# Kernel tuning notes

Measured on AMD Instinct MI355X. Metric: run time of the kernel, lower is better.

Reference implementation:

```python
import jax, jax.numpy as jnp
import numpy as np

N = 50000
E = 800000
H = 128

def _mlp_params(key, sizes, biases):
    # sizes: list of (in, out); biases: list of bool
    params = []
    for i, ((fi, fo), b) in enumerate(zip(sizes, biases)):
        k = jax.random.fold_in(key, i)
        bound = 1.0 / np.sqrt(fi)
        W = jax.random.uniform(k, (fi, fo), minval=-bound, maxval=bound, dtype=jnp.float32)
        if b:
            bb = jax.random.uniform(jax.random.fold_in(k, 7), (fo,), minval=-bound, maxval=bound, dtype=jnp.float32)
        else:
            bb = None
        params.append((W, bb))
    return params

def setup_inputs() -> dict:
    key = jax.random.key(0)
    ks = jax.random.split(key, 8)
    h = jax.random.normal(ks[0], (N, H), dtype=jnp.float32)
    pos = jax.random.normal(ks[1], (N, 3), dtype=jnp.float32)
    edge_index = jax.random.randint(ks[2], (2, E), 0, N, dtype=jnp.int32)
    edge_p = _mlp_params(ks[3], [(2 * H + 1, H), (H, H)], [True, True])
    node_p = _mlp_params(ks[4], [(2 * H, H), (H, H)], [True, True])
    coord_p = _mlp_params(ks[5], [(H, H), (H, 1)], [True, False])
    return {
        'h': h, 'pos': pos, 'edge_index': edge_index,
        'eW0': edge_p[0][0], 'eb0': edge_p[0][1], 'eW1': edge_p[1][0], 'eb1': edge_p[1][1],
        'nW0': node_p[0][0], 'nb0': node_p[0][1], 'nW1': node_p[1][0], 'nb1': node_p[1][1],
        'cW0': coord_p[0][0], 'cb0': coord_p[0][1], 'cW1': coord_p[1][0],
    }

def reference(h, pos, edge_index, eW0, eb0, eW1, eb1, nW0, nb0, nW1, nb1, cW0, cb0, cW1):
    row, col = edge_index[0], edge_index[1]
    coord_diff = pos[row] - pos[col]                         # [E, 3]
    radial = jnp.sum(coord_diff ** 2, axis=1, keepdims=True)  # [E, 1]
    edge_feat = jnp.concatenate([h[row], h[col], radial], axis=1)  # [E, 2H+1]
    # edge MLP: Linear -> SiLU -> Linear -> SiLU
    m_ij = jax.nn.silu(edge_feat @ eW0 + eb0)
    m_ij = jax.nn.silu(m_ij @ eW1 + eb1)                     # [E, H]
    # coord MLP: Linear -> SiLU -> Linear(no bias)
    coord_weight = jax.nn.silu(m_ij @ cW0 + cb0) @ cW1       # [E, 1]
    norm = jnp.sqrt(radial + 1e-8)
    coord_update = coord_diff / norm * coord_weight          # [E, 3]
    # scatter-add messages to target nodes
    m_i = jax.ops.segment_sum(m_ij, row, num_segments=h.shape[0])
    node_in = jnp.concatenate([h, m_i], axis=1)              # [N, 2H]
    h_new = h + jax.nn.silu(node_in @ nW0 + nb0) @ nW1 + nb1
    pos_update = jax.ops.segment_sum(coord_update, row, num_segments=pos.shape[0])
    deg = jax.ops.segment_sum(jnp.ones((row.shape[0],), jnp.float32), row, num_segments=pos.shape[0])
    pos_new = pos + pos_update / (deg[:, None] + 1e-6)
    return h_new, pos_new
```

## Files before the change

kernel.cpp:

```cpp
#include <hip/hip_runtime.h>
#include <hip/hip_bf16.h>
#include <cstddef>

#define N_NODES 50000
#define N_EDGES 800000
#define HDIM    128
#define TME     64
#define TMN     64

#define RB128   272
#define RB256   528

#define SCHUNK  512
#define SNBLK   ((N_NODES + SCHUNK - 1) / SCHUNK)

typedef __attribute__((ext_vector_type(4))) float f32x4;
typedef __attribute__((ext_vector_type(8))) short bf16x8;

#define OFF_EW0T 0
#define OFF_EW0B 16384
#define OFF_EW1  32768
#define OFF_CW0  49152
#define OFF_NW0  65536
#define OFF_NW1  98304
#define PACK_ELEMS 114688

__device__ __forceinline__ float silu(float x) {
    float e = __expf(-x);
    return __fdividef(x, 1.0f + e);
}
__device__ __forceinline__ unsigned short f2bf(float f) {
    union { __hip_bfloat16 h; unsigned short u; } cv;
    cv.h = __float2bfloat16(f);
    return cv.u;
}
__device__ __forceinline__ unsigned int f2bf2(float a, float b) {
    union { __hip_bfloat162 h; unsigned int u; } cv;
    cv.h = __float22bfloat162_rn(float2{a, b});
    return cv.u;
}
__device__ __forceinline__ float bf2f(unsigned short u) {
    return __uint_as_float(((unsigned int)u) << 16);
}
__device__ __forceinline__ float bflo(unsigned int u) {
    return __uint_as_float(u << 16);
}
__device__ __forceinline__ float bfhi(unsigned int u) {
    return __uint_as_float(u & 0xffff0000u);
}

__global__ void pack_weights(const float* __restrict__ eW0, const float* __restrict__ eW1,
                             const float* __restrict__ cW0, const float* __restrict__ nW0,
                             const float* __restrict__ nW1, unsigned short* __restrict__ pack)
{
    int g = blockIdx.x * blockDim.x + threadIdx.x;
    int f = g >> 6;
    int lane = g & 63;
    const float* W; int base; int rowoff = 0;
    if (f < 32)       { W = eW0; base = OFF_EW0T; }
    else if (f < 64)  { W = eW0; base = OFF_EW0B; f -= 32; rowoff = 128; }
    else if (f < 96)  { W = eW1; base = OFF_EW1;  f -= 64; }
    else if (f < 128) { W = cW0; base = OFF_CW0;  f -= 96; }
    else if (f < 192) { W = nW0; base = OFF_NW0;  f -= 128; }
    else              { W = nW1; base = OFF_NW1;  f -= 192; }
    int KS = (base == OFF_NW0) ? 8 : 4;
    int cb = f / KS, ks = f % KS;
    int col = cb * 16 + (lane & 15);
    int kbase = rowoff + ks * 32 + ((lane >> 4) << 3);
#pragma unroll
    for (int j = 0; j < 8; ++j)
        pack[(size_t)base + ((size_t)(f * 64 + lane) * 8 + j)] =
            f2bf(W[(size_t)(kbase + j) * HDIM + col]);
}

__global__ __launch_bounds__(256)
void scanA_kernel(const int* __restrict__ cnt, int* __restrict__ bsum) {
    __shared__ int part[256];
    const int b = blockIdx.x, t = threadIdx.x;
    int i0 = b * SCHUNK + t * 2;
    int s = 0;
    if (i0 < N_NODES)     s += cnt[i0];
    if (i0 + 1 < N_NODES) s += cnt[i0 + 1];
    part[t] = s;
    __syncthreads();
    for (int off = 128; off > 0; off >>= 1) {
        if (t < off) part[t] += part[t + off];
        __syncthreads();
    }
    if (t == 0) bsum[b] = part[0];
}

__global__ __launch_bounds__(128)
void scanB_kernel(const int* __restrict__ bsum, int* __restrict__ boff,
                  int* __restrict__ row_start) {
    __shared__ int part[128];
    const int t = threadIdx.x;
    int s = (t < SNBLK) ? bsum[t] : 0;
    part[t] = s;
    __syncthreads();
    for (int off = 1; off < 128; off <<= 1) {
        int tmp = (t >= off) ? part[t - off] : 0;
        __syncthreads();
        part[t] += tmp;
        __syncthreads();
    }
    boff[t] = part[t] - s;
    if (t == 127) row_start[N_NODES] = part[127];
}

__global__ __launch_bounds__(256)
void scanC_kernel(const int* __restrict__ cnt, const int* __restrict__ boff,
                  int* __restrict__ row_start, int* __restrict__ cursor) {
    __shared__ int part[256];
    const int b = blockIdx.x, t = threadIdx.x;
    int i0 = b * SCHUNK + t * 2;
    int c0 = (i0 < N_NODES) ? cnt[i0] : 0;
    int c1 = (i0 + 1 < N_NODES) ? cnt[i0 + 1] : 0;
    int s = c0 + c1;
    part[t] = s;
    __syncthreads();
    for (int off = 1; off < 256; off <<= 1) {
        int tmp = (t >= off) ? part[t - off] : 0;
        __syncthreads();
        part[t] += tmp;
        __syncthreads();
    }
    int base = boff[b] + part[t] - s;
    if (i0 < N_NODES)     { row_start[i0] = base;          cursor[i0] = base; }
    if (i0 + 1 < N_NODES) { row_start[i0 + 1] = base + c0; cursor[i0 + 1] = base + c0; }
}

__global__ void scatter_kernel(const int* __restrict__ eidx, int* __restrict__ cursor,
                               int2* __restrict__ rc) {
    int e = (blockIdx.x * blockDim.x + threadIdx.x) * 4;
    if (e + 3 < N_EDGES) {
        int4 r4 = *(const int4*)(eidx + e);
        int4 c4 = *(const int4*)(eidx + N_EDGES + e);
        int p;
        p = atomicAdd(&cursor[r4.x], 1); rc[p] = int2{r4.x, c4.x};
        p = atomicAdd(&cursor[r4.y], 1); rc[p] = int2{r4.y, c4.y};
        p = atomicAdd(&cursor[r4.z], 1); rc[p] = int2{r4.z, c4.z};
        p = atomicAdd(&cursor[r4.w], 1); rc[p] = int2{r4.w, c4.w};
    } else {
        for (int i = e; i < N_EDGES; ++i) {
            int r = eidx[i], c = eidx[N_EDGES + i];
            int p = atomicAdd(&cursor[r], 1);
            rc[p] = int2{r, c};
        }
    }
}

template<int KS, int ROWB>
__device__ __forceinline__ void gemm_layer_T(const unsigned short* __restrict__ Wseg,
                                             const char* __restrict__ Xs,
                                             int lane, int cb, f32x4 acc[4])
{
    const bf16x8* aptr = (const bf16x8*)Wseg + (size_t)(cb * KS) * 64 + lane;
#pragma unroll
    for (int ks = 0; ks < KS; ++ks) {
        bf16x8 a = aptr[(size_t)ks * 64];
#pragma unroll
        for (int eb = 0; eb < 4; ++eb) {
            int row = eb * 16 + (lane & 15);
            bf16x8 b = *(const bf16x8*)(Xs + row * ROWB + ks * 64 + ((lane >> 4) << 4));
            acc[eb] = __builtin_amdgcn_mfma_f32_16x16x32_bf16(a, b, acc[eb], 0, 0, 0);
        }
    }
}

__global__ __launch_bounds__(512, 2)
void h0_kernel(const float* __restrict__ h, const float* __restrict__ eb0,
               const unsigned short* __restrict__ pack,
               const int* __restrict__ eidx, int* __restrict__ cnt,
               unsigned short* __restrict__ H0r, unsigned short* __restrict__ H0c)
{
    __shared__ __align__(16) char Xs[TMN * RB128];
    const int tid = threadIdx.x, lane = tid & 63, cb = tid >> 6;
    const int n0 = blockIdx.x * TMN;

    {
        int e = blockIdx.x * 1024 + tid * 2;
        if (e + 1 < N_EDGES) {
            int2 rr = *(const int2*)(eidx + e);
            atomicAdd(&cnt[rr.x], 1);
            atomicAdd(&cnt[rr.y], 1);
        } else if (e < N_EDGES) {
            atomicAdd(&cnt[eidx[e]], 1);
        }
    }

    {
        const int nl = tid >> 3, sub = tid & 7, n = n0 + nl;
        if (n < N_NODES) {
            const float4* h4 = (const float4*)(h + (size_t)n * HDIM);
#pragma unroll
            for (int q = 0; q < 4; ++q) {
                float4 f = h4[sub + q * 8];
                uint2 u; u.x = f2bf2(f.x, f.y); u.y = f2bf2(f.z, f.w);
                *(uint2*)(Xs + nl * RB128 + (sub + q * 8) * 8) = u;
            }
        } else {
            uint2 z{0, 0};
#pragma unroll
            for (int q = 0; q < 4; ++q)
                *(uint2*)(Xs + nl * RB128 + (sub + q * 8) * 8) = z;
        }
    }
    __syncthreads();

    const int j0 = cb * 16 + ((lane >> 4) << 2);
    f32x4 acc[4];
    {
        float4 b0 = *(const float4*)(eb0 + j0);
#pragma unroll
        for (int eb = 0; eb < 4; ++eb) acc[eb] = f32x4{b0.x, b0.y, b0.z, b0.w};
        gemm_layer_T<4, RB128>(pack + OFF_EW0T, Xs, lane, cb, acc);
#pragma unroll
        for (int eb = 0; eb < 4; ++eb) {
            int n = n0 + eb * 16 + (lane & 15);
            if (n < N_NODES) {
                uint2 u; u.x = f2bf2(acc[eb][0], acc[eb][1]); u.y = f2bf2(acc[eb][2], acc[eb][3]);
                *(uint2*)(H0r + (size_t)n * HDIM + j0) = u;
            }
        }
    }
    {
#pragma unroll
        for (int eb = 0; eb < 4; ++eb) acc[eb] = f32x4{0.f, 0.f, 0.f, 0.f};
        gemm_layer_T<4, RB128>(pack + OFF_EW0B, Xs, lane, cb, acc);
#pragma unroll
        for (int eb = 0; eb < 4; ++eb) {
            int n = n0 + eb * 16 + (lane & 15);
            if (n < N_NODES) {
                uint2 u; u.x = f2bf2(acc[eb][0], acc[eb][1]); u.y = f2bf2(acc[eb][2], acc[eb][3]);
                *(uint2*)(H0c + (size_t)n * HDIM + j0) = u;
            }
        }
    }
}

__global__ __launch_bounds__(512, 4)
void egnn_edge_kernel(const unsigned short* __restrict__ H0r,
                      const unsigned short* __restrict__ H0c,
                      const float* __restrict__ pos,
                      const int2*  __restrict__ rc,
                      const float* __restrict__ w256,
                      const float* __restrict__ eb1, const float* __restrict__ cb0,
                      const float* __restrict__ cW1,
                      const unsigned short* __restrict__ pack,
                      float* __restrict__ m_i,
                      float* __restrict__ pos_upd)
{
    __shared__ __align__(16) char Ya[TME * RB128];
    __shared__ __align__(16) char Yb[TME * RB128];
    __shared__ float pw[8][TME];
    __shared__ float rad_s[TME];
    __shared__ float dif_s[TME][3];
    __shared__ float cu_s[TME][4];
    __shared__ int   rowb_s[TME];

    const int tid = threadIdx.x, lane = tid & 63, cb = tid >> 6;

    int lb;
    {
        const int nwg = gridDim.x;
        const int q = nwg >> 3, r = nwg & 7;
        const int xcd = blockIdx.x & 7, idx = blockIdx.x >> 3;
        lb = (xcd < r) ? (xcd * (q + 1) + idx) : (r * (q + 1) + (xcd - r) * q + idx);
    }
    const int e0 = lb * TME;

    {
        const int el = tid >> 3, sub = tid & 7, idx = e0 + el;
        const int2 rcv = rc[idx];
        const int r = rcv.x, c = rcv.y;
        float dx = pos[(size_t)r * 3 + 0] - pos[(size_t)c * 3 + 0];
        float dy = pos[(size_t)r * 3 + 1] - pos[(size_t)c * 3 + 1];
        float dz = pos[(size_t)r * 3 + 2] - pos[(size_t)c * 3 + 2];
        float rad = dx * dx + dy * dy + dz * dz;
        if (sub == 0) {
            rad_s[el] = rad;
            dif_s[el][0] = dx; dif_s[el][1] = dy; dif_s[el][2] = dz;
            rowb_s[el] = r;
        }
        const bf16x8* ar = (const bf16x8*)(H0r + (size_t)r * HDIM + sub * 16);
        const bf16x8* ac = (const bf16x8*)(H0c + (size_t)c * HDIM + sub * 16);
        bf16x8 a0 = ar[0], a1 = ar[1];
        bf16x8 c0 = ac[0], c1 = ac[1];
        const float4* wp = (const float4*)(w256 + sub * 16);
        float4 w4[4] = { wp[0], wp[1], wp[2], wp[3] };
        const float* wf = (const float*)w4;
        float v[16];
#pragma unroll
        for (int i = 0; i < 8; ++i) v[i]     = bf2f((unsigned short)a0[i]) + bf2f((unsigned short)c0[i]);
#pragma unroll
        for (int i = 0; i < 8; ++i) v[8 + i] = bf2f((unsigned short)a1[i]) + bf2f((unsigned short)c1[i]);
#pragma unroll
        for (int i = 0; i < 16; ++i) v[i] = silu(fmaf(rad, wf[i], v[i]));
#pragma unroll
        for (int c4 = 0; c4 < 4; ++c4) {
            uint2 u;
            u.x = f2bf2(v[c4 * 4 + 0], v[c4 * 4 + 1]);
            u.y = f2bf2(v[c4 * 4 + 2], v[c4 * 4 + 3]);
            *(uint2*)(Ya + el * RB128 + sub * 32 + c4 * 8) = u;
        }
    }
    __syncthreads();

    const int j0 = cb * 16 + ((lane >> 4) << 2);
    f32x4 acc[4];

    {
        float4 b1 = *(const float4*)(eb1 + j0);
#pragma unroll
        for (int eb = 0; eb < 4; ++eb) acc[eb] = f32x4{b1.x, b1.y, b1.z, b1.w};
        gemm_layer_T<4, RB128>(pack + OFF_EW1, Ya, lane, cb, acc);
#pragma unroll
        for (int eb = 0; eb < 4; ++eb) {
            int e = eb * 16 + (lane & 15);
            float s0 = silu(acc[eb][0]), s1 = silu(acc[eb][1]);
            float s2 = silu(acc[eb][2]), s3 = silu(acc[eb][3]);
            uint2 u; u.x = f2bf2(s0, s1); u.y = f2bf2(s2, s3);
            *(uint2*)(Yb + e * RB128 + j0 * 2) = u;
        }
    }
    __syncthreads();

    {
        const int rcol = tid & 127;
        const int ch   = tid >> 7;
        float run = 0.f;
        int cur = rowb_s[ch * 16];
#pragma unroll
        for (int i = 0; i < 16; ++i) {
            int row = ch * 16 + i;
            int rr = rowb_s[row];
            if (rr != cur) {
                atomicAdd(&m_i[(size_t)cur * HDIM + rcol], run);
                run = 0.f; cur = rr;
            }
            unsigned short u = *(const unsigned short*)(Yb + row * RB128 + rcol * 2);
            run += bf2f(u);
        }
        atomicAdd(&m_i[(size_t)cur * HDIM + rcol], run);
    }

    {
        float4 b2 = *(const float4*)(cb0 + j0);
#pragma unroll
        for (int eb = 0; eb < 4; ++eb) acc[eb] = f32x4{b2.x, b2.y, b2.z, b2.w};
        gemm_layer_T<4, RB128>(pack + OFF_CW0, Yb, lane, cb, acc);
        float4 w1 = *(const float4*)(cW1 + j0);
        float pe[4];
#pragma unroll
        for (int eb = 0; eb < 4; ++eb) {
            float p;
            p = silu(acc[eb][0]) * w1.x;
            p = fmaf(silu(acc[eb][1]), w1.y, p);
            p = fmaf(silu(acc[eb][2]), w1.z, p);
            p = fmaf(silu(acc[eb][3]), w1.w, p);
            p += __shfl_xor(p, 16);
            p += __shfl_xor(p, 32);
            pe[eb] = p;
        }
        if (lane < 16) {
#pragma unroll
            for (int eb = 0; eb < 4; ++eb) pw[cb][eb * 16 + lane] = pe[eb];
        }
    }
    __syncthreads();

    if (tid < TME) {
        float s = 0.f;
#pragma unroll
        for (int w = 0; w < 8; ++w) s += pw[w][tid];
        float inv = 1.0f / sqrtf(rad_s[tid] + 1e-8f);
        float cwv = s * inv;
        cu_s[tid][0] = dif_s[tid][0] * cwv;
        cu_s[tid][1] = dif_s[tid][1] * cwv;
        cu_s[tid][2] = dif_s[tid][2] * cwv;
    }
    __syncthreads();

    if (tid < TME) {
        const int el = tid;
        bool head = (el == 0) || (rowb_s[el] != rowb_s[el - 1]);
        if (head) {
            float sx = 0.f, sy = 0.f, sz = 0.f;
            int r = rowb_s[el];
            int j = el;
            do {
                sx += cu_s[j][0]; sy += cu_s[j][1]; sz += cu_s[j][2];
                ++j;
            } while (j < TME && rowb_s[j] == r);
            atomicAdd(&pos_upd[(size_t)r * 3 + 0], sx);
            atomicAdd(&pos_upd[(size_t)r * 3 + 1], sy);
            atomicAdd(&pos_upd[(size_t)r * 3 + 2], sz);
        }
    }
}

__global__ __launch_bounds__(512)
void egnn_node_kernel(const float* __restrict__ h,
                      const float* __restrict__ pos,
                      const float* __restrict__ m_i,
                      const float* __restrict__ pos_upd,
                      const int*   __restrict__ row_start,
                      const float* __restrict__ nb0, const float* __restrict__ nb1,
                      const unsigned short* __restrict__ pack,
                      float* __restrict__ out_h,
                      float* __restrict__ out_pos)
{
    __shared__ __align__(16) char Xs[TMN * RB256];
    __shared__ __align__(16) char Ya[TMN * RB128];

    const int tid = threadIdx.x, lane = tid & 63, cb = tid >> 6;
    const int n0 = blockIdx.x * TMN;

    if (tid < TMN * 3) {
        int nl = tid / 3, d = tid % 3;
        int n = n0 + nl;
        if (n < N_NODES) {
            float dv = (float)(row_start[n + 1] - row_start[n]);
            out_pos[(size_t)n * 3 + d] =
                pos[(size_t)n * 3 + d] + pos_upd[(size_t)n * 3 + d] / (dv + 1e-6f);
        }
    }

    {
        const int nl = tid >> 3, sub = tid & 7, n = n0 + nl;
        if (n < N_NODES) {
            const float4* h4 = (const float4*)(h   + (size_t)n * HDIM);
            const float4* m4 = (const float4*)(m_i + (size_t)n * HDIM);
#pragma unroll
            for (int q = 0; q < 4; ++q) {
                float4 fh = h4[sub + q * 8];
                float4 fm = m4[sub + q * 8];
                uint2 uh; uh.x = f2bf2(fh.x, fh.y); uh.y = f2bf2(fh.z, fh.w);
                uint2 um; um.x = f2bf2(fm.x, fm.y); um.y = f2bf2(fm.z, fm.w);
                *(uint2*)(Xs + nl * RB256 + (sub + q * 8) * 8)       = uh;
                *(uint2*)(Xs + nl * RB256 + 256 + (sub + q * 8) * 8) = um;
            }
        } else {
            uint2 z{0, 0};
#pragma unroll
            for (int q = 0; q < 4; ++q) {
                *(uint2*)(Xs + nl * RB256 + (sub + q * 8) * 8)       = z;
                *(uint2*)(Xs + nl * RB256 + 256 + (sub + q * 8) * 8) = z;
            }
        }
    }
    __syncthreads();

    const int j0 = cb * 16 + ((lane >> 4) << 2);
    f32x4 acc[4];

    {
        float4 b0 = *(const float4*)(nb0 + j0);
#pragma unroll
        for (int eb = 0; eb < 4; ++eb) acc[eb] = f32x4{b0.x, b0.y, b0.z, b0.w};
        gemm_layer_T<8, RB256>(pack + OFF_NW0, Xs, lane, cb, acc);
#pragma unroll
        for (int eb = 0; eb < 4; ++eb) {
            int nl = eb * 16 + (lane & 15);
            float s0 = silu(acc[eb][0]), s1 = silu(acc[eb][1]);
            float s2 = silu(acc[eb][2]), s3 = silu(acc[eb][3]);
            uint2 u; u.x = f2bf2(s0, s1); u.y = f2bf2(s2, s3);
            *(uint2*)(Ya + nl * RB128 + j0 * 2) = u;
        }
    }
    __syncthreads();

    {
        float4 b1 = *(const float4*)(nb1 + j0);
#pragma unroll
        for (int eb = 0; eb < 4; ++eb) acc[eb] = f32x4{b1.x, b1.y, b1.z, b1.w};
        gemm_layer_T<4, RB128>(pack + OFF_NW1, Ya, lane, cb, acc);
#pragma unroll
        for (int eb = 0; eb < 4; ++eb) {
            int n = n0 + eb * 16 + (lane & 15);
            if (n < N_NODES) {
                float4 hv = *(const float4*)(h + (size_t)n * HDIM + j0);
                float4 o;
                o.x = hv.x + acc[eb][0]; o.y = hv.y + acc[eb][1];
                o.z = hv.z + acc[eb][2]; o.w = hv.w + acc[eb][3];
                *(float4*)(out_h + (size_t)n * HDIM + j0) = o;
            }
        }
    }
}

extern "C" void kernel_launch(void* const* d_in, const int* in_sizes, int n_in,
                              void* d_out, int out_size, void* d_ws, size_t ws_size,
                              hipStream_t stream) {
    const float* h    = (const float*)d_in[0];
    const float* pos  = (const float*)d_in[1];
    const int*   eidx = (const int*)  d_in[2];
    const float* eW0  = (const float*)d_in[3];
    const float* eb0  = (const float*)d_in[4];
    const float* eW1  = (const float*)d_in[5];
    const float* eb1  = (const float*)d_in[6];
    const float* nW0  = (const float*)d_in[7];
    const float* nb0  = (const float*)d_in[8];
    const float* nW1  = (const float*)d_in[9];
    const float* nb1  = (const float*)d_in[10];
    const float* cW0  = (const float*)d_in[11];
    const float* cb0  = (const float*)d_in[12];
    const float* cW1  = (const float*)d_in[13];

    float* out_h   = (float*)d_out;
    float* out_pos = out_h + (size_t)N_NODES * HDIM;

    float* m_i       = (float*)d_ws;
    float* pos_upd   = m_i + (size_t)N_NODES * HDIM;
    int*   cnt       = (int*)(pos_upd + (size_t)N_NODES * 3);
    int*   row_start = cnt + N_NODES;
    int*   cursor    = row_start + N_NODES + 1;
    int*   bsum      = cursor + N_NODES;
    int*   boff      = bsum + 128;
    int2*  rc        = (int2*)(boff + 128);
    unsigned short* pack = (unsigned short*)(rc + N_EDGES);
    unsigned short* H0r  = pack + PACK_ELEMS;
    unsigned short* H0c  = H0r + (size_t)N_NODES * HDIM;

    size_t zero_bytes = ((size_t)N_NODES * HDIM + (size_t)N_NODES * 3 + N_NODES) * sizeof(float);
    hipMemsetAsync(m_i, 0, zero_bytes, stream);

    pack_weights<<<56, 256, 0, stream>>>(eW0, eW1, cW0, nW0, nW1, pack);

    h0_kernel<<<(N_NODES + TMN - 1) / TMN, 512, 0, stream>>>(h, eb0, pack, eidx, cnt, H0r, H0c);

    scanA_kernel<<<SNBLK, 256, 0, stream>>>(cnt, bsum);
    scanB_kernel<<<1, 128, 0, stream>>>(bsum, boff, row_start);
    scanC_kernel<<<SNBLK, 256, 0, stream>>>(cnt, boff, row_start, cursor);
    scatter_kernel<<<(N_EDGES / 4 + 255) / 256, 256, 0, stream>>>(eidx, cursor, rc);

    egnn_edge_kernel<<<N_EDGES / TME, 512, 0, stream>>>(
        H0r, H0c, pos, rc, eW0 + (size_t)256 * HDIM, eb1, cb0, cW1,
        pack, m_i, pos_upd);

    egnn_node_kernel<<<(N_NODES + TMN - 1) / TMN, 512, 0, stream>>>(
        h, pos, m_i, pos_upd, row_start, nb0, nb1, pack, out_h, out_pos);
}
```

Before: 338.5 us.

## Switch GEMMs to 32x32x16 MFMA tiles and precompute node h-part in h0 kernel

```diff
diff --git a/kernel.cpp b/kernel.cpp
--- a/kernel.cpp
+++ b/kernel.cpp
@@ -9,19 +9,20 @@
 #define TMN     64
 
 #define RB128   272
-#define RB256   528
 
 #define SCHUNK  512
 #define SNBLK   ((N_NODES + SCHUNK - 1) / SCHUNK)
 
-typedef __attribute__((ext_vector_type(4))) float f32x4;
-typedef __attribute__((ext_vector_type(8))) short bf16x8;
+typedef __attribute__((ext_vector_type(4)))  float f32x4;
+typedef __attribute__((ext_vector_type(16))) float f32x16;
+typedef __attribute__((ext_vector_type(8)))  short bf16x8;
 
 #define OFF_EW0T 0
 #define OFF_EW0B 16384
 #define OFF_EW1  32768
 #define OFF_CW0  49152
-#define OFF_NW0  65536
+#define OFF_NW0T 65536
+#define OFF_NW0B 81920
 #define OFF_NW1  98304
 #define PACK_ELEMS 114688
 
@@ -54,23 +55,28 @@
                              const float* __restrict__ nW1, unsigned short* __restrict__ pack)
 {
     int g = blockIdx.x * blockDim.x + threadIdx.x;
-    int f = g >> 6;
+    int fg = g >> 6;
     int lane = g & 63;
-    const float* W; int base; int rowoff = 0;
-    if (f < 32)       { W = eW0; base = OFF_EW0T; }
-    else if (f < 64)  { W = eW0; base = OFF_EW0B; f -= 32; rowoff = 128; }
-    else if (f < 96)  { W = eW1; base = OFF_EW1;  f -= 64; }
-    else if (f < 128) { W = cW0; base = OFF_CW0;  f -= 96; }
-    else if (f < 192) { W = nW0; base = OFF_NW0;  f -= 128; }
-    else              { W = nW1; base = OFF_NW1;  f -= 192; }
-    int KS = (base == OFF_NW0) ? 8 : 4;
-    int cb = f / KS, ks = f % KS;
-    int col = cb * 16 + (lane & 15);
-    int kbase = rowoff + ks * 32 + ((lane >> 4) << 3);
-#pragma unroll
-    for (int j = 0; j < 8; ++j)
-        pack[(size_t)base + ((size_t)(f * 64 + lane) * 8 + j)] =
-            f2bf(W[(size_t)(kbase + j) * HDIM + col]);
+    int s = fg >> 5;
+    int f = fg & 31;
+    const float* W; int rowoff = 0;
+    switch (s) {
+        case 0: W = eW0; break;
+        case 1: W = eW0; rowoff = 128; break;
+        case 2: W = eW1; break;
+        case 3: W = cW0; break;
+        case 4: W = nW0; break;
+        case 5: W = nW0; rowoff = 128; break;
+        default: W = nW1; break;
+    }
+    int base = s * 16384;
+    int cb = f >> 3, ks = f & 7;
+    int col = cb * 32 + (lane & 31);
+    int kbase = rowoff + ks * 16 + ((lane >> 5) << 3);
+#pragma unroll
+    for (int q = 0; q < 8; ++q)
+        pack[(size_t)base + ((size_t)(f * 64 + lane) * 8 + q)] =
+            f2bf(W[(size_t)(kbase + q) * HDIM + col]);
 }
 
 __global__ __launch_bounds__(256)
@@ -150,32 +156,34 @@
     }
 }
 
-template<int KS, int ROWB>
-__device__ __forceinline__ void gemm_layer_T(const unsigned short* __restrict__ Wseg,
-                                             const char* __restrict__ Xs,
-                                             int lane, int cb, f32x4 acc[4])
+template<int ROWB>
+__device__ __forceinline__ void gemm32(const unsigned short* __restrict__ Wseg,
+                                       const char* __restrict__ Xs,
+                                       int lane, int cbw, int ebk, f32x16& acc)
 {
-    const bf16x8* aptr = (const bf16x8*)Wseg + (size_t)(cb * KS) * 64 + lane;
-#pragma unroll
-    for (int ks = 0; ks < KS; ++ks) {
+    const bf16x8* aptr = (const bf16x8*)Wseg + (size_t)(cbw * 8) * 64 + lane;
+    const char* xrow = Xs + (ebk * 32 + (lane & 31)) * ROWB + ((lane >> 5) << 4);
+#pragma unroll
+    for (int ks = 0; ks < 8; ++ks) {
         bf16x8 a = aptr[(size_t)ks * 64];
-#pragma unroll
-        for (int eb = 0; eb < 4; ++eb) {
-            int row = eb * 16 + (lane & 15);
-            bf16x8 b = *(const bf16x8*)(Xs + row * ROWB + ks * 64 + ((lane >> 4) << 4));
-            acc[eb] = __builtin_amdgcn_mfma_f32_16x16x32_bf16(a, b, acc[eb], 0, 0, 0);
-        }
-    }
-}
+        bf16x8 b = *(const bf16x8*)(xrow + ks * 32);
+        acc = __builtin_amdgcn_mfma_f32_32x32x16_bf16(a, b, acc, 0, 0, 0);
+    }
+}
+
+#define F0(rq) (cbw * 32 + (rq) * 8 + ((lane >> 5) << 2))
 
 __global__ __launch_bounds__(512, 2)
 void h0_kernel(const float* __restrict__ h, const float* __restrict__ eb0,
+               const float* __restrict__ nb0,
                const unsigned short* __restrict__ pack,
                const int* __restrict__ eidx, int* __restrict__ cnt,
-               unsigned short* __restrict__ H0r, unsigned short* __restrict__ H0c)
+               unsigned short* __restrict__ H0r, unsigned short* __restrict__ H0c,
+               unsigned short* __restrict__ Hn0)
 {
     __shared__ __align__(16) char Xs[TMN * RB128];
-    const int tid = threadIdx.x, lane = tid & 63, cb = tid >> 6;
+    const int tid = threadIdx.x, lane = tid & 63, wv = tid >> 6;
+    const int cbw = wv & 3, ebk = wv >> 2;
     const int n0 = blockIdx.x * TMN;
 
     {
@@ -208,32 +216,57 @@
     }
     __syncthreads();
 
-    const int j0 = cb * 16 + ((lane >> 4) << 2);
-    f32x4 acc[4];
-    {
-        float4 b0 = *(const float4*)(eb0 + j0);
-#pragma unroll
-        for (int eb = 0; eb < 4; ++eb) acc[eb] = f32x4{b0.x, b0.y, b0.z, b0.w};
-        gemm_layer_T<4, RB128>(pack + OFF_EW0T, Xs, lane, cb, acc);
-#pragma unroll
-        for (int eb = 0; eb < 4; ++eb) {
-            int n = n0 + eb * 16 + (lane & 15);
-            if (n < N_NODES) {
-                uint2 u; u.x = f2bf2(acc[eb][0], acc[eb][1]); u.y = f2bf2(acc[eb][2], acc[eb][3]);
-                *(uint2*)(H0r + (size_t)n * HDIM + j0) = u;
-            }
-        }
-    }
-    {
-#pragma unroll
-        for (int eb = 0; eb < 4; ++eb) acc[eb] = f32x4{0.f, 0.f, 0.f, 0.f};
-        gemm_layer_T<4, RB128>(pack + OFF_EW0B, Xs, lane, cb, acc);
-#pragma unroll
-        for (int eb = 0; eb < 4; ++eb) {
-            int n = n0 + eb * 16 + (lane & 15);
-            if (n < N_NODES) {
-                uint2 u; u.x = f2bf2(acc[eb][0], acc[eb][1]); u.y = f2bf2(acc[eb][2], acc[eb][3]);
-                *(uint2*)(H0c + (size_t)n * HDIM + j0) = u;
+    const int e_loc = ebk * 32 + (lane & 31);
+    const int n = n0 + e_loc;
+    f32x16 acc;
+
+    {
+#pragma unroll
+        for (int rq = 0; rq < 4; ++rq) {
+            float4 b = *(const float4*)(eb0 + F0(rq));
+            acc[rq * 4 + 0] = b.x; acc[rq * 4 + 1] = b.y;
+            acc[rq * 4 + 2] = b.z; acc[rq * 4 + 3] = b.w;
+        }
+        gemm32<RB128>(pack + OFF_EW0T, Xs, lane, cbw, ebk, acc);
+        if (n < N_NODES) {
+#pragma unroll
+            for (int rq = 0; rq < 4; ++rq) {
+                uint2 u;
+                u.x = f2bf2(acc[rq * 4 + 0], acc[rq * 4 + 1]);
+                u.y = f2bf2(acc[rq * 4 + 2], acc[rq * 4 + 3]);
+                *(uint2*)(H0r + (size_t)n * HDIM + F0(rq)) = u;
+            }
+        }
+    }
+    {
+#pragma unroll
+        for (int i = 0; i < 16; ++i) acc[i] = 0.f;
+        gemm32<RB128>(pack + OFF_EW0B, Xs, lane, cbw, ebk, acc);
+        if (n < N_NODES) {
+#pragma unroll
+            for (int rq = 0; rq < 4; ++rq) {
+                uint2 u;
+                u.x = f2bf2(acc[rq * 4 + 0], acc[rq * 4 + 1]);
+                u.y = f2bf2(acc[rq * 4 + 2], acc[rq * 4 + 3]);
+                *(uint2*)(H0c + (size_t)n * HDIM + F0(rq)) = u;
+            }
+        }
+    }
+    {
+#pragma unroll
+        for (int rq = 0; rq < 4; ++rq) {
+            float4 b = *(const float4*)(nb0 + F0(rq));
+            acc[rq * 4 + 0] = b.x; acc[rq * 4 + 1] = b.y;
+            acc[rq * 4 + 2] = b.z; acc[rq * 4 + 3] = b.w;
+        }
+        gemm32<RB128>(pack + OFF_NW0T, Xs, lane, cbw, ebk, acc);
+        if (n < N_NODES) {
+#pragma unroll
+            for (int rq = 0; rq < 4; ++rq) {
+                uint2 u;
+                u.x = f2bf2(acc[rq * 4 + 0], acc[rq * 4 + 1]);
+                u.y = f2bf2(acc[rq * 4 + 2], acc[rq * 4 + 3]);
+                *(uint2*)(Hn0 + (size_t)n * HDIM + F0(rq)) = u;
             }
         }
     }
@@ -253,13 +286,14 @@
 {
     __shared__ __align__(16) char Ya[TME * RB128];
     __shared__ __align__(16) char Yb[TME * RB128];
-    __shared__ float pw[8][TME];
+    __shared__ float pw[4][TME];
     __shared__ float rad_s[TME];
     __shared__ float dif_s[TME][3];
     __shared__ float cu_s[TME][4];
     __shared__ int   rowb_s[TME];
 
-    const int tid = threadIdx.x, lane = tid & 63, cb = tid >> 6;
+    const int tid = threadIdx.x, lane = tid & 63, wv = tid >> 6;
+    const int cbw = wv & 3, ebk = wv >> 2;
 
     int lb;
     {
@@ -307,21 +341,23 @@
     }
     __syncthreads();
 
-    const int j0 = cb * 16 + ((lane >> 4) << 2);
-    f32x4 acc[4];
-
-    {
-        float4 b1 = *(const float4*)(eb1 + j0);
-#pragma unroll
-        for (int eb = 0; eb < 4; ++eb) acc[eb] = f32x4{b1.x, b1.y, b1.z, b1.w};
-        gemm_layer_T<4, RB128>(pack + OFF_EW1, Ya, lane, cb, acc);
-#pragma unroll
-        for (int eb = 0; eb < 4; ++eb) {
-            int e = eb * 16 + (lane & 15);
-            float s0 = silu(acc[eb][0]), s1 = silu(acc[eb][1]);
-            float s2 = silu(acc[eb][2]), s3 = silu(acc[eb][3]);
+    const int e_loc = ebk * 32 + (lane & 31);
+    f32x16 acc;
+
+    {
+#pragma unroll
+        for (int rq = 0; rq < 4; ++rq) {
+            float4 b = *(const float4*)(eb1 + F0(rq));
+            acc[rq * 4 + 0] = b.x; acc[rq * 4 + 1] = b.y;
+            acc[rq * 4 + 2] = b.z; acc[rq * 4 + 3] = b.w;
+        }
+        gemm32<RB128>(pack + OFF_EW1, Ya, lane, cbw, ebk, acc);
+#pragma unroll
+        for (int rq = 0; rq < 4; ++rq) {
+            float s0 = silu(acc[rq * 4 + 0]), s1 = silu(acc[rq * 4 + 1]);
+            float s2 = silu(acc[rq * 4 + 2]), s3 = silu(acc[rq * 4 + 3]);
             uint2 u; u.x = f2bf2(s0, s1); u.y = f2bf2(s2, s3);
-            *(uint2*)(Yb + e * RB128 + j0 * 2) = u;
+            *(uint2*)(Yb + e_loc * RB128 + F0(rq) * 2) = u;
         }
     }
     __syncthreads();
@@ -346,34 +382,29 @@
     }
 
     {
-        float4 b2 = *(const float4*)(cb0 + j0);
-#pragma unroll
-        for (int eb = 0; eb < 4; ++eb) acc[eb] = f32x4{b2.x, b2.y, b2.z, b2.w};
-        gemm_layer_T<4, RB128>(pack + OFF_CW0, Yb, lane, cb, acc);
-        float4 w1 = *(const float4*)(cW1 + j0);
-        float pe[4];
-#pragma unroll
-        for (int eb = 0; eb < 4; ++eb) {
-            float p;
-            p = silu(acc[eb][0]) * w1.x;
-            p = fmaf(silu(acc[eb][1]), w1.y, p);
-            p = fmaf(silu(acc[eb][2]), w1.z, p);
-            p = fmaf(silu(acc[eb][3]), w1.w, p);
-            p += __shfl_xor(p, 16);
-            p += __shfl_xor(p, 32);
-            pe[eb] = p;
-        }
-        if (lane < 16) {
-#pragma unroll
-            for (int eb = 0; eb < 4; ++eb) pw[cb][eb * 16 + lane] = pe[eb];
-        }
+#pragma unroll
+        for (int rq = 0; rq < 4; ++rq) {
+            float4 b = *(const float4*)(cb0 + F0(rq));
+            acc[rq * 4 + 0] = b.x; acc[rq * 4 + 1] = b.y;
+            acc[rq * 4 + 2] = b.z; acc[rq * 4 + 3] = b.w;
+        }
+        gemm32<RB128>(pack + OFF_CW0, Yb, lane, cbw, ebk, acc);
+        float p = 0.f;
+#pragma unroll
+        for (int rq = 0; rq < 4; ++rq) {
+            float4 w1 = *(const float4*)(cW1 + F0(rq));
+            p = fmaf(silu(acc[rq * 4 + 0]), w1.x, p);
+            p = fmaf(silu(acc[rq * 4 + 1]), w1.y, p);
+            p = fmaf(silu(acc[rq * 4 + 2]), w1.z, p);
+            p = fmaf(silu(acc[rq * 4 + 3]), w1.w, p);
+        }
+        p += __shfl_xor(p, 32);
+        if (lane < 32) pw[cbw][ebk * 32 + lane] = p;
     }
     __syncthreads();
 
     if (tid < TME) {
-        float s = 0.f;
-#pragma unroll
-        for (int w = 0; w < 8; ++w) s += pw[w][tid];
+        float s = pw[0][tid] + pw[1][tid] + pw[2][tid] + pw[3][tid];
         float inv = 1.0f / sqrtf(rad_s[tid] + 1e-8f);
         float cwv = s * inv;
         cu_s[tid][0] = dif_s[tid][0] * cwv;
@@ -406,15 +437,17 @@
                       const float* __restrict__ m_i,
                       const float* __restrict__ pos_upd,
                       const int*   __restrict__ row_start,
-                      const float* __restrict__ nb0, const float* __restrict__ nb1,
+                      const unsigned short* __restrict__ Hn0,
+                      const float* __restrict__ nb1,
                       const unsigned short* __restrict__ pack,
                       float* __restrict__ out_h,
                       float* __restrict__ out_pos)
 {
-    __shared__ __align__(16) char Xs[TMN * RB256];
+    __shared__ __align__(16) char Xs[TMN * RB128];
     __shared__ __align__(16) char Ya[TMN * RB128];
 
-    const int tid = threadIdx.x, lane = tid & 63, cb = tid >> 6;
+    const int tid = threadIdx.x, lane = tid & 63, wv = tid >> 6;
+    const int cbw = wv & 3, ebk = wv >> 2;
     const int n0 = blockIdx.x * TMN;
 
     if (tid < TMN * 3) {
@@ -430,61 +463,65 @@
     {
         const int nl = tid >> 3, sub = tid & 7, n = n0 + nl;
         if (n < N_NODES) {
-            const float4* h4 = (const float4*)(h   + (size_t)n * HDIM);
             const float4* m4 = (const float4*)(m_i + (size_t)n * HDIM);
 #pragma unroll
             for (int q = 0; q < 4; ++q) {
-                float4 fh = h4[sub + q * 8];
                 float4 fm = m4[sub + q * 8];
-                uint2 uh; uh.x = f2bf2(fh.x, fh.y); uh.y = f2bf2(fh.z, fh.w);
                 uint2 um; um.x = f2bf2(fm.x, fm.y); um.y = f2bf2(fm.z, fm.w);
-                *(uint2*)(Xs + nl * RB256 + (sub + q * 8) * 8)       = uh;
-                *(uint2*)(Xs + nl * RB256 + 256 + (sub + q * 8) * 8) = um;
+                *(uint2*)(Xs + nl * RB128 + (sub + q * 8) * 8) = um;
             }
         } else {
             uint2 z{0, 0};
 #pragma unroll
-            for (int q = 0; q < 4; ++q) {
-                *(uint2*)(Xs + nl * RB256 + (sub + q * 8) * 8)       = z;
-                *(uint2*)(Xs + nl * RB256 + 256 + (sub + q * 8) * 8) = z;
-            }
-        }
-    }
-    __syncthreads();
-
-    const int j0 = cb * 16 + ((lane >> 4) << 2);
-    f32x4 acc[4];
-
-    {
-        float4 b0 = *(const float4*)(nb0 + j0);
-#pragma unroll
-        for (int eb = 0; eb < 4; ++eb) acc[eb] = f32x4{b0.x, b0.y, b0.z, b0.w};
-        gemm_layer_T<8, RB256>(pack + OFF_NW0, Xs, lane, cb, acc);
-#pragma unroll
-        for (int eb = 0; eb < 4; ++eb) {
-            int nl = eb * 16 + (lane & 15);
-            float s0 = silu(acc[eb][0]), s1 = silu(acc[eb][1]);
-            float s2 = silu(acc[eb][2]), s3 = silu(acc[eb][3]);
+            for (int q = 0; q < 4; ++q)
+                *(uint2*)(Xs + nl * RB128 + (sub + q * 8) * 8) = z;
+        }
+    }
+    __syncthreads();
+
+    const int e_loc = ebk * 32 + (lane & 31);
+    const int n = n0 + e_loc;
+    f32x16 acc;
+
+    {
+        if (n < N_NODES) {
+#pragma unroll
+            for (int rq = 0; rq < 4; ++rq) {
+                uint2 u = *(const uint2*)(Hn0 + (size_t)n * HDIM + F0(rq));
+                acc[rq * 4 + 0] = bflo(u.x); acc[rq * 4 + 1] = bfhi(u.x);
+                acc[rq * 4 + 2] = bflo(u.y); acc[rq * 4 + 3] = bfhi(u.y);
+            }
+        } else {
+#pragma unroll
+            for (int i = 0; i < 16; ++i) acc[i] = 0.f;
+        }
+        gemm32<RB128>(pack + OFF_NW0B, Xs, lane, cbw, ebk, acc);
+#pragma unroll
+        for (int rq = 0; rq < 4; ++rq) {
+            float s0 = silu(acc[rq * 4 + 0]), s1 = silu(acc[rq * 4 + 1]);
+            float s2 = silu(acc[rq * 4 + 2]), s3 = silu(acc[rq * 4 + 3]);
             uint2 u; u.x = f2bf2(s0, s1); u.y = f2bf2(s2, s3);
-            *(uint2*)(Ya + nl * RB128 + j0 * 2) = u;
-        }
-    }
-    __syncthreads();
-
-    {
-        float4 b1 = *(const float4*)(nb1 + j0);
-#pragma unroll
-        for (int eb = 0; eb < 4; ++eb) acc[eb] = f32x4{b1.x, b1.y, b1.z, b1.w};
-        gemm_layer_T<4, RB128>(pack + OFF_NW1, Ya, lane, cb, acc);
-#pragma unroll
-        for (int eb = 0; eb < 4; ++eb) {
-            int n = n0 + eb * 16 + (lane & 15);
-            if (n < N_NODES) {
-                float4 hv = *(const float4*)(h + (size_t)n * HDIM + j0);
+            *(uint2*)(Ya + e_loc * RB128 + F0(rq) * 2) = u;
+        }
+    }
+    __syncthreads();
+
+    {
+#pragma unroll
+        for (int rq = 0; rq < 4; ++rq) {
+            float4 b = *(const float4*)(nb1 + F0(rq));
+            acc[rq * 4 + 0] = b.x; acc[rq * 4 + 1] = b.y;
+            acc[rq * 4 + 2] = b.z; acc[rq * 4 + 3] = b.w;
+        }
+        gemm32<RB128>(pack + OFF_NW1, Ya, lane, cbw, ebk, acc);
+        if (n < N_NODES) {
+#pragma unroll
+            for (int rq = 0; rq < 4; ++rq) {
+                float4 hv = *(const float4*)(h + (size_t)n * HDIM + F0(rq));
                 float4 o;
-                o.x = hv.x + acc[eb][0]; o.y = hv.y + acc[eb][1];
-                o.z = hv.z + acc[eb][2]; o.w = hv.w + acc[eb][3];
-                *(float4*)(out_h + (size_t)n * HDIM + j0) = o;
+                o.x = hv.x + acc[rq * 4 + 0]; o.y = hv.y + acc[rq * 4 + 1];
+                o.z = hv.z + acc[rq * 4 + 2]; o.w = hv.w + acc[rq * 4 + 3];
+                *(float4*)(out_h + (size_t)n * HDIM + F0(rq)) = o;
             }
         }
     }
@@ -522,13 +559,15 @@
     unsigned short* pack = (unsigned short*)(rc + N_EDGES);
     unsigned short* H0r  = pack + PACK_ELEMS;
     unsigned short* H0c  = H0r + (size_t)N_NODES * HDIM;
+    unsigned short* Hn0  = H0c + (size_t)N_NODES * HDIM;
 
     size_t zero_bytes = ((size_t)N_NODES * HDIM + (size_t)N_NODES * 3 + N_NODES) * sizeof(float);
     hipMemsetAsync(m_i, 0, zero_bytes, stream);
 
     pack_weights<<<56, 256, 0, stream>>>(eW0, eW1, cW0, nW0, nW1, pack);
 
-    h0_kernel<<<(N_NODES + TMN - 1) / TMN, 512, 0, stream>>>(h, eb0, pack, eidx, cnt, H0r, H0c);
+    h0_kernel<<<(N_NODES + TMN - 1) / TMN, 512, 0, stream>>>(
+        h, eb0, nb0, pack, eidx, cnt, H0r, H0c, Hn0);
 
     scanA_kernel<<<SNBLK, 256, 0, stream>>>(cnt, bsum);
     scanB_kernel<<<1, 128, 0, stream>>>(bsum, boff, row_start);
@@ -540,5 +579,5 @@
         pack, m_i, pos_upd);
 
     egnn_node_kernel<<<(N_NODES + TMN - 1) / TMN, 512, 0, stream>>>(
-        h, pos, m_i, pos_upd, row_start, nb0, nb1, pack, out_h, out_pos);
-}
+        h, pos, m_i, pos_upd, row_start, Hn0, nb1, pack, out_h, out_pos);
+}
```

Result: slower. 374.8 us (+10.7%).

## Precompute h·nW0 top half in h0 kernel and make segment row uniform

Applied to the files above, without the earlier changes.

```diff
diff --git a/kernel.cpp b/kernel.cpp
--- a/kernel.cpp
+++ b/kernel.cpp
@@ -9,7 +9,6 @@
 #define TMN     64
 
 #define RB128   272
-#define RB256   528
 
 #define SCHUNK  512
 #define SNBLK   ((N_NODES + SCHUNK - 1) / SCHUNK)
@@ -21,7 +20,8 @@
 #define OFF_EW0B 16384
 #define OFF_EW1  32768
 #define OFF_CW0  49152
-#define OFF_NW0  65536
+#define OFF_NW0T 65536
+#define OFF_NW0B 81920
 #define OFF_NW1  98304
 #define PACK_ELEMS 114688
 
@@ -54,17 +54,22 @@
                              const float* __restrict__ nW1, unsigned short* __restrict__ pack)
 {
     int g = blockIdx.x * blockDim.x + threadIdx.x;
-    int f = g >> 6;
+    int fg = g >> 6;
     int lane = g & 63;
-    const float* W; int base; int rowoff = 0;
-    if (f < 32)       { W = eW0; base = OFF_EW0T; }
-    else if (f < 64)  { W = eW0; base = OFF_EW0B; f -= 32; rowoff = 128; }
-    else if (f < 96)  { W = eW1; base = OFF_EW1;  f -= 64; }
-    else if (f < 128) { W = cW0; base = OFF_CW0;  f -= 96; }
-    else if (f < 192) { W = nW0; base = OFF_NW0;  f -= 128; }
-    else              { W = nW1; base = OFF_NW1;  f -= 192; }
-    int KS = (base == OFF_NW0) ? 8 : 4;
-    int cb = f / KS, ks = f % KS;
+    int s = fg >> 5;
+    int f = fg & 31;
+    const float* W; int rowoff = 0;
+    switch (s) {
+        case 0: W = eW0; break;
+        case 1: W = eW0; rowoff = 128; break;
+        case 2: W = eW1; break;
+        case 3: W = cW0; break;
+        case 4: W = nW0; break;
+        case 5: W = nW0; rowoff = 128; break;
+        default: W = nW1; break;
+    }
+    int base = s * 16384;
+    int cb = f >> 2, ks = f & 3;
     int col = cb * 16 + (lane & 15);
     int kbase = rowoff + ks * 32 + ((lane >> 4) << 3);
 #pragma unroll
@@ -170,9 +175,11 @@
 
 __global__ __launch_bounds__(512, 2)
 void h0_kernel(const float* __restrict__ h, const float* __restrict__ eb0,
+               const float* __restrict__ nb0,
                const unsigned short* __restrict__ pack,
                const int* __restrict__ eidx, int* __restrict__ cnt,
-               unsigned short* __restrict__ H0r, unsigned short* __restrict__ H0c)
+               unsigned short* __restrict__ H0r, unsigned short* __restrict__ H0c,
+               unsigned short* __restrict__ Hn0)
 {
     __shared__ __align__(16) char Xs[TMN * RB128];
     const int tid = threadIdx.x, lane = tid & 63, cb = tid >> 6;
@@ -234,6 +241,20 @@
             if (n < N_NODES) {
                 uint2 u; u.x = f2bf2(acc[eb][0], acc[eb][1]); u.y = f2bf2(acc[eb][2], acc[eb][3]);
                 *(uint2*)(H0c + (size_t)n * HDIM + j0) = u;
+            }
+        }
+    }
+    {
+        float4 b0 = *(const float4*)(nb0 + j0);
+#pragma unroll
+        for (int eb = 0; eb < 4; ++eb) acc[eb] = f32x4{b0.x, b0.y, b0.z, b0.w};
+        gemm_layer_T<4, RB128>(pack + OFF_NW0T, Xs, lane, cb, acc);
+#pragma unroll
+        for (int eb = 0; eb < 4; ++eb) {
+            int n = n0 + eb * 16 + (lane & 15);
+            if (n < N_NODES) {
+                uint2 u; u.x = f2bf2(acc[eb][0], acc[eb][1]); u.y = f2bf2(acc[eb][2], acc[eb][3]);
+                *(uint2*)(Hn0 + (size_t)n * HDIM + j0) = u;
             }
         }
     }
@@ -330,11 +351,11 @@
         const int rcol = tid & 127;
         const int ch   = tid >> 7;
         float run = 0.f;
-        int cur = rowb_s[ch * 16];
+        int cur = __builtin_amdgcn_readfirstlane(rowb_s[ch * 16]);
 #pragma unroll
         for (int i = 0; i < 16; ++i) {
             int row = ch * 16 + i;
-            int rr = rowb_s[row];
+            int rr = __builtin_amdgcn_readfirstlane(rowb_s[row]);
             if (rr != cur) {
                 atomicAdd(&m_i[(size_t)cur * HDIM + rcol], run);
                 run = 0.f; cur = rr;
@@ -406,12 +427,13 @@
                       const float* __restrict__ m_i,
                       const float* __restrict__ pos_upd,
                       const int*   __restrict__ row_start,
-                      const float* __restrict__ nb0, const float* __restrict__ nb1,
+                      const unsigned short* __restrict__ Hn0,
+                      const float* __restrict__ nb1,
                       const unsigned short* __restrict__ pack,
                       float* __restrict__ out_h,
                       float* __restrict__ out_pos)
 {
-    __shared__ __align__(16) char Xs[TMN * RB256];
+    __shared__ __align__(16) char Xs[TMN * RB128];
     __shared__ __align__(16) char Ya[TMN * RB128];
 
     const int tid = threadIdx.x, lane = tid & 63, cb = tid >> 6;
@@ -430,24 +452,18 @@
     {
         const int nl = tid >> 3, sub = tid & 7, n = n0 + nl;
         if (n < N_NODES) {
-            const float4* h4 = (const float4*)(h   + (size_t)n * HDIM);
             const float4* m4 = (const float4*)(m_i + (size_t)n * HDIM);
 #pragma unroll
             for (int q = 0; q < 4; ++q) {
-                float4 fh = h4[sub + q * 8];
                 float4 fm = m4[sub + q * 8];
-                uint2 uh; uh.x = f2bf2(fh.x, fh.y); uh.y = f2bf2(fh.z, fh.w);
                 uint2 um; um.x = f2bf2(fm.x, fm.y); um.y = f2bf2(fm.z, fm.w);
-                *(uint2*)(Xs + nl * RB256 + (sub + q * 8) * 8)       = uh;
-                *(uint2*)(Xs + nl * RB256 + 256 + (sub + q * 8) * 8) = um;
+                *(uint2*)(Xs + nl * RB128 + (sub + q * 8) * 8) = um;
             }
         } else {
             uint2 z{0, 0};
 #pragma unroll
-            for (int q = 0; q < 4; ++q) {
-                *(uint2*)(Xs + nl * RB256 + (sub + q * 8) * 8)       = z;
-                *(uint2*)(Xs + nl * RB256 + 256 + (sub + q * 8) * 8) = z;
-            }
+            for (int q = 0; q < 4; ++q)
+                *(uint2*)(Xs + nl * RB128 + (sub + q * 8) * 8) = z;
         }
     }
     __syncthreads();
@@ -456,10 +472,17 @@
     f32x4 acc[4];
 
     {
-        float4 b0 = *(const float4*)(nb0 + j0);
-#pragma unroll
-        for (int eb = 0; eb < 4; ++eb) acc[eb] = f32x4{b0.x, b0.y, b0.z, b0.w};
-        gemm_layer_T<8, RB256>(pack + OFF_NW0, Xs, lane, cb, acc);
+#pragma unroll
+        for (int eb = 0; eb < 4; ++eb) {
+            int n = n0 + eb * 16 + (lane & 15);
+            if (n < N_NODES) {
+                uint2 u = *(const uint2*)(Hn0 + (size_t)n * HDIM + j0);
+                acc[eb] = f32x4{bflo(u.x), bfhi(u.x), bflo(u.y), bfhi(u.y)};
+            } else {
+                acc[eb] = f32x4{0.f, 0.f, 0.f, 0.f};
+            }
+        }
+        gemm_layer_T<4, RB128>(pack + OFF_NW0B, Xs, lane, cb, acc);
 #pragma unroll
         for (int eb = 0; eb < 4; ++eb) {
             int nl = eb * 16 + (lane & 15);
@@ -522,13 +545,15 @@
     unsigned short* pack = (unsigned short*)(rc + N_EDGES);
     unsigned short* H0r  = pack + PACK_ELEMS;
     unsigned short* H0c  = H0r + (size_t)N_NODES * HDIM;
+    unsigned short* Hn0  = H0c + (size_t)N_NODES * HDIM;
 
     size_t zero_bytes = ((size_t)N_NODES * HDIM + (size_t)N_NODES * 3 + N_NODES) * sizeof(float);
     hipMemsetAsync(m_i, 0, zero_bytes, stream);
 
     pack_weights<<<56, 256, 0, stream>>>(eW0, eW1, cW0, nW0, nW1, pack);
 
-    h0_kernel<<<(N_NODES + TMN - 1) / TMN, 512, 0, stream>>>(h, eb0, pack, eidx, cnt, H0r, H0c);
+    h0_kernel<<<(N_NODES + TMN - 1) / TMN, 512, 0, stream>>>(
+        h, eb0, nb0, pack, eidx, cnt, H0r, H0c, Hn0);
 
     scanA_kernel<<<SNBLK, 256, 0, stream>>>(cnt, bsum);
     scanB_kernel<<<1, 128, 0, stream>>>(bsum, boff, row_start);
@@ -540,5 +565,5 @@
         pack, m_i, pos_upd);
 
     egnn_node_kernel<<<(N_NODES + TMN - 1) / TMN, 512, 0, stream>>>(
-        h, pos, m_i, pos_upd, row_start, nb0, nb1, pack, out_h, out_pos);
-}
+        h, pos, m_i, pos_upd, row_start, Hn0, nb1, pack, out_h, out_pos);
+}
```

Measured after the change: 341.6 us. About the same (+0.9%).
